# Kernel tuning notes

Hardware: AMD Instinct MI355X
Metric: run time of the kernel (lower is better)

The kernel has to match this reference:

```python
import jax, jax.numpy as jnp
import numpy as np

EPS = 1e-5
N_NODES = 50000


def batchnorm(x, gamma, beta):
    # training-mode BatchNorm1d: batch mean, biased variance
    mean = jnp.mean(x, axis=0)
    var = jnp.mean(jnp.square(x - mean), axis=0)
    return (x - mean) * jax.lax.rsqrt(var + EPS) * gamma + beta


def setup_inputs() -> dict:
    key = jax.random.key(0)
    ks = jax.random.split(key, 8)
    N, E, D_IN, D_H, D_OUT = N_NODES, 800000, 128, 128, 128
    feat = jax.random.normal(ks[0], (N, D_IN), dtype=jnp.float32)
    w = jax.random.uniform(ks[1], (E,), dtype=jnp.float32)
    # xavier_uniform with relu gain for Q and W
    gain = float(np.sqrt(2.0))
    bq = gain * np.sqrt(6.0 / (D_IN + D_H))
    bw = gain * np.sqrt(6.0 / (D_IN + D_H + D_OUT))
    Q_w = jax.random.uniform(ks[2], (D_H, D_IN), minval=-bq, maxval=bq, dtype=jnp.float32)
    W_w = jax.random.uniform(ks[3], (D_OUT, D_IN + D_H), minval=-bw, maxval=bw, dtype=jnp.float32)
    Q_b = jnp.zeros((D_H,), jnp.float32)
    W_b = jnp.zeros((D_OUT,), jnp.float32)
    gamma2 = jnp.ones((D_OUT,), jnp.float32)
    beta2 = jnp.zeros((D_OUT,), jnp.float32)
    src = jax.random.randint(ks[4], (E,), 0, N, dtype=jnp.int32)
    dst = jax.random.randint(ks[5], (E,), 0, N, dtype=jnp.int32)
    return {"feat": feat, "w": w, "Q_w": Q_w, "Q_b": Q_b, "W_w": W_w,
            "W_b": W_b, "gamma2": gamma2, "beta2": beta2, "src": src, "dst": dst}


def reference(feat, w, Q_w, Q_b, W_w, W_b, gamma2, beta2, src, dst):
    N = feat.shape[0]
    # h = dropout(bnorm_two(relu(Q(feat))))  (dropout=0 -> identity; source reuses bnorm_two)
    h = batchnorm(jax.nn.relu(feat @ Q_w.T + Q_b), gamma2, beta2)  # [N, H]
    # weighted neighbor mean: sum_e w_e * h[src_e] scattered to dst, / sum_e w_e
    num = jax.ops.segment_sum(w[:, None] * h[src], dst, num_segments=N)  # [N, H]
    den = jax.ops.segment_sum(w, dst, num_segments=N)  # [N]
    has_msg = den[:, None] != 0
    agg = jnp.where(has_msg, num / jnp.where(has_msg, den[:, None], 1.0), h)
    rst = jnp.concatenate([feat, agg], axis=1) @ W_w.T + W_b  # [N, OUT]
    rst = batchnorm(jax.nn.relu(rst), gamma2, beta2)
    denom = jnp.linalg.norm(rst, axis=1, keepdims=True)
    return rst / jnp.where(denom == 0, 1.0, denom)
```

## Files before the change

kernel.cpp:

```cpp
#include <hip/hip_runtime.h>
#include <stdint.h>


#define BN_EPS 1e-5f
#define NSLOT 32

typedef __attribute__((ext_vector_type(8))) short bf16x8;
typedef __attribute__((ext_vector_type(4))) float f32x4;

static __device__ __forceinline__ unsigned short f2bf(float f) {
    uint32_t u = __builtin_bit_cast(uint32_t, f);
    u += 0x7fffu + ((u >> 16) & 1u);
    return (unsigned short)(u >> 16);
}
static __device__ __forceinline__ float bf_lo(uint32_t u) {
    return __builtin_bit_cast(float, u << 16);
}
static __device__ __forceinline__ float bf_hi(uint32_t u) {
    return __builtin_bit_cast(float, u & 0xffff0000u);
}

__global__ __launch_bounds__(256) void k_pre(
    const float* __restrict__ feat, unsigned short* __restrict__ featb, int nf,
    const int* __restrict__ dst, int* __restrict__ ccnt, int E, int CB)
{
    if ((int)blockIdx.x < CB) {
        int i = (blockIdx.x * 256 + threadIdx.x) * 4;
        if (i + 3 < nf) {
            float4 v = *(const float4*)(feat + i);
            ushort4 o;
            o.x = f2bf(v.x); o.y = f2bf(v.y); o.z = f2bf(v.z); o.w = f2bf(v.w);
            *(ushort4*)(featb + i) = o;
        } else {
            for (int j = i; j < nf; ++j) featb[j] = f2bf(feat[j]);
        }
    } else {
        __shared__ int hcnt[128];
        const int tid = threadIdx.x;
        if (tid < 128) hcnt[tid] = 0;
        __syncthreads();
        const int base_e = (blockIdx.x - CB) * 2048;
#pragma unroll
        for (int j = 0; j < 8; ++j) {
            int e = base_e + j * 256 + tid;
            if (e < E) atomicAdd(&hcnt[dst[e] >> 9], 1);
        }
        __syncthreads();
        if (tid < 128 && hcnt[tid] > 0) atomicAdd(&ccnt[tid], hcnt[tid]);
    }
}

__global__ __launch_bounds__(128) void k_coffs(
    const int* __restrict__ ccnt, int* __restrict__ coffs,
    int* __restrict__ gcur, int* __restrict__ offs, int N, int E)
{
    __shared__ int w0sum;
    const int t = threadIdx.x;
    const int lane = t & 63, wv = t >> 6;
    int v = ccnt[t];
    int incl = v;
#pragma unroll
    for (int o = 1; o < 64; o <<= 1) {
        int u = __shfl_up(incl, o, 64);
        if (lane >= o) incl += u;
    }
    if (wv == 0 && lane == 63) w0sum = incl;
    __syncthreads();
    int excl = incl - v + (wv ? w0sum : 0);
    coffs[t] = excl;
    gcur[t]  = excl;
    if (t == 127) { coffs[128] = excl + v; offs[N] = E; }
}

template<int K>
static __device__ __forceinline__ void gemm_body(
    int bid,
    const unsigned short* __restrict__ A_lo,
    const unsigned short* __restrict__ A_hi,
    const float* __restrict__ B,
    const float* __restrict__ bias,
    float* __restrict__ Y,
    double* __restrict__ sum, double* __restrict__ sumsq, int N)
{
    constexpr int SA = 72;
    __shared__ unsigned short As[64 * SA];
    __shared__ unsigned short Bs[128 * SA];
    __shared__ float bsum_s[128], bsq_s[128];

    const int tid  = threadIdx.x;
    const int lane = tid & 63;
    const int wv   = tid >> 6;
    const int wr   = wv >> 1;
    const int wc   = wv & 1;
    const int m15  = lane & 15;
    const int quad = lane >> 4;
    const int r0   = bid * 64;

    if (tid < 128) { bsum_s[tid] = 0.f; bsq_s[tid] = 0.f; }

    f32x4 acc[2][4];
#pragma unroll
    for (int rt = 0; rt < 2; ++rt)
#pragma unroll
        for (int ct = 0; ct < 4; ++ct)
            acc[rt][ct] = (f32x4){0.f, 0.f, 0.f, 0.f};

    for (int kc = 0; kc < K; kc += 64) {
        const unsigned short* Ap = (kc < 128) ? A_lo : A_hi;
        const int koff = kc & 127;
#pragma unroll
        for (int i = 0; i < 2; ++i) {
            int idx = i * 256 + tid;
            int row = idx >> 3, seg = idx & 7;
            int gr  = r0 + row; if (gr >= N) gr = N - 1;
            uint4 v = *(const uint4*)(Ap + (size_t)gr * 128 + koff + seg * 8);
            *(uint4*)(As + row * SA + seg * 8) = v;
        }
#pragma unroll
        for (int i = 0; i < 8; ++i) {
            int idx = i * 256 + tid;
            int row = idx >> 4, seg = idx & 15;
            float4 v = *(const float4*)(B + (size_t)row * K + kc + seg * 4);
            ushort4 o;
            o.x = f2bf(v.x); o.y = f2bf(v.y); o.z = f2bf(v.z); o.w = f2bf(v.w);
            *(ushort4*)(Bs + row * SA + seg * 4) = o;
        }
        __syncthreads();

#pragma unroll
        for (int ks = 0; ks < 64; ks += 32) {
            bf16x8 af[2], bfr[4];
#pragma unroll
            for (int rt = 0; rt < 2; ++rt)
                af[rt] = *(const bf16x8*)(As + (wr * 32 + rt * 16 + m15) * SA + ks + quad * 8);
#pragma unroll
            for (int ct = 0; ct < 4; ++ct)
                bfr[ct] = *(const bf16x8*)(Bs + (wc * 64 + ct * 16 + m15) * SA + ks + quad * 8);
#pragma unroll
            for (int rt = 0; rt < 2; ++rt)
#pragma unroll
                for (int ct = 0; ct < 4; ++ct)
                    acc[rt][ct] = __builtin_amdgcn_mfma_f32_16x16x32_bf16(
                        af[rt], bfr[ct], acc[rt][ct], 0, 0, 0);
        }
        __syncthreads();
    }

#pragma unroll
    for (int ct = 0; ct < 4; ++ct) {
        int col = wc * 64 + ct * 16 + m15;
        float bz = bias[col];
        float s = 0.f, q = 0.f;
#pragma unroll
        for (int rt = 0; rt < 2; ++rt) {
#pragma unroll
            for (int reg = 0; reg < 4; ++reg) {
                int row = r0 + wr * 32 + rt * 16 + quad * 4 + reg;
                float v = fmaxf(acc[rt][ct][reg] + bz, 0.f);
                if (row < N) {
                    Y[(size_t)row * 128 + col] = v;
                } else {
                    v = 0.f;
                }
                s += v; q = fmaf(v, v, q);
            }
        }
        s += __shfl_xor(s, 16, 64); s += __shfl_xor(s, 32, 64);
        q += __shfl_xor(q, 16, 64); q += __shfl_xor(q, 32, 64);
        if (quad == 0) {
            atomicAdd(&bsum_s[col], s);
            atomicAdd(&bsq_s[col], q);
        }
    }
    __syncthreads();
    if (tid < 128) {
        const int slot = (bid & (NSLOT - 1)) * 128;
        atomicAdd(&sum[slot + tid],   (double)bsum_s[tid]);
        atomicAdd(&sumsq[slot + tid], (double)bsq_s[tid]);
    }
}

static __device__ __forceinline__ void bin_body(
    int bid,
    const int* __restrict__ src, const int* __restrict__ dst,
    const float* __restrict__ w, int* __restrict__ gcur,
    int4* __restrict__ tmp, int E)
{
    __shared__ int hcnt[128];
    __shared__ int hbase[128];
    const int tid = threadIdx.x;
    if (tid < 128) hcnt[tid] = 0;
    __syncthreads();

    int d8[8], s8[8], slot8[8];
    float w8[8];
#pragma unroll
    for (int j = 0; j < 8; ++j) {
        int e = bid * 2048 + j * 256 + tid;
        if (e < E) {
            d8[j] = dst[e]; s8[j] = src[e]; w8[j] = w[e];
            slot8[j] = atomicAdd(&hcnt[d8[j] >> 9], 1);
        } else d8[j] = -1;
    }
    __syncthreads();
    if (tid < 128 && hcnt[tid] > 0)
        hbase[tid] = atomicAdd(&gcur[tid], hcnt[tid]);
    __syncthreads();
#pragma unroll
    for (int j = 0; j < 8; ++j) {
        if (d8[j] >= 0) {
            int pos = hbase[d8[j] >> 9] + slot8[j];
            tmp[pos] = make_int4(s8[j], __float_as_int(w8[j]), d8[j], 0);
        }
    }
}

__global__ __launch_bounds__(256) void k_bin_gemm(
    const int* __restrict__ src, const int* __restrict__ dst,
    const float* __restrict__ w, int* __restrict__ gcur,
    int4* __restrict__ tmp, int E, int HB,
    const unsigned short* __restrict__ featb,
    const float* __restrict__ Qw, const float* __restrict__ Qb,
    float* __restrict__ y1,
    double* __restrict__ sum, double* __restrict__ sumsq, int N)
{
    if ((int)blockIdx.x < HB)
        bin_body(blockIdx.x, src, dst, w, gcur, tmp, E);
    else
        gemm_body<128>(blockIdx.x - HB, featb, featb, Qw, Qb, y1, sum, sumsq, N);
}

__global__ __launch_bounds__(128) void bn_coef(
    const double* __restrict__ sum, const double* __restrict__ sumsq,
    const float* __restrict__ gamma, const float* __restrict__ beta,
    float* __restrict__ a, float* __restrict__ b, double invN)
{
    const int t = threadIdx.x;
    double ms = 0.0, qs = 0.0;
#pragma unroll
    for (int s = 0; s < NSLOT; ++s) {
        ms += sum[s * 128 + t];
        qs += sumsq[s * 128 + t];
    }
    float mean = (float)(ms * invN);
    float var  = (float)(qs * invN) - mean * mean;
    float sc = rsqrtf(var + BN_EPS) * gamma[t];
    a[t] = sc;
    b[t] = fmaf(-mean, sc, beta[t]);
}

static __device__ __forceinline__ void refine_body(
    int b,
    const int4* __restrict__ tmp, const int* __restrict__ coffs,
    int* __restrict__ offs, int2* __restrict__ epack, int N)
{
    __shared__ int hist[512];
    __shared__ int wpre[4];
    const int d0   = b << 9;
    const int dlim = min(512, N - d0);
    const int tid  = threadIdx.x;
    const int lane = tid & 63, wv = tid >> 6;
    const int start = coffs[b];
    const int end   = coffs[b + 1];

    hist[tid] = 0; hist[tid + 256] = 0;
    __syncthreads();

    for (int p = start + tid; p < end; p += 256)
        atomicAdd(&hist[tmp[p].z - d0], 1);
    __syncthreads();

    int v0 = hist[2 * tid], v1 = hist[2 * tid + 1];
    int s = v0 + v1;
    int incl = s;
#pragma unroll
    for (int o = 1; o < 64; o <<= 1) {
        int t = __shfl_up(incl, o, 64);
        if (lane >= o) incl += t;
    }
    if (lane == 63) wpre[wv] = incl;
    __syncthreads();
    if (tid == 0) {
        int r = 0;
#pragma unroll
        for (int i = 0; i < 4; ++i) { int t = wpre[i]; wpre[i] = r; r += t; }
    }
    __syncthreads();
    int e0 = start + wpre[wv] + incl - s;
    if (2 * tid < dlim)     offs[d0 + 2 * tid]     = e0;
    if (2 * tid + 1 < dlim) offs[d0 + 2 * tid + 1] = e0 + v0;
    hist[2 * tid]     = e0;
    hist[2 * tid + 1] = e0 + v0;
    __syncthreads();

    for (int p = start + tid; p < end; p += 256) {
        int4 rec = tmp[p];
        int pos = atomicAdd(&hist[rec.z - d0], 1);
        epack[pos] = make_int2(rec.x, rec.y);
    }
}

__global__ __launch_bounds__(256) void k_refine_apply(
    const int4* __restrict__ tmp, const int* __restrict__ coffs,
    int* __restrict__ offs, int2* __restrict__ epack, int N, int NB,
    const float* __restrict__ y,
    const float* __restrict__ a, const float* __restrict__ b,
    unsigned short* __restrict__ h, int n)
{
    if ((int)blockIdx.x < NB) {
        refine_body(blockIdx.x, tmp, coffs, offs, epack, N);
    } else {
        int i = ((blockIdx.x - NB) * 256 + threadIdx.x) * 4;
        if (i >= n) return;
        int c = i & 127;
        float4 v  = *(const float4*)(y + i);
        float4 av = *(const float4*)(a + c);
        float4 bv = *(const float4*)(b + c);
        ushort4 o;
        o.x = f2bf(fmaf(av.x, v.x, bv.x));
        o.y = f2bf(fmaf(av.y, v.y, bv.y));
        o.z = f2bf(fmaf(av.z, v.z, bv.z));
        o.w = f2bf(fmaf(av.w, v.w, bv.w));
        *(ushort4*)(h + i) = o;
    }
}

__global__ __launch_bounds__(256) void gather_agg(
    const unsigned short* __restrict__ h,
    const int* __restrict__ offs, const int2* __restrict__ epack,
    unsigned short* __restrict__ aggb, int N)
{
    const int r    = (int)((blockIdx.x * 256u + threadIdx.x) >> 6);
    const int lane = threadIdx.x & 63;
    if (r >= N) return;
    int p = offs[r];
    const int end = offs[r + 1];
    float nx = 0.f, ny = 0.f, den = 0.f;
    for (; p + 3 < end; p += 4) {
        int2 e0 = epack[p],     e1 = epack[p + 1];
        int2 e2 = epack[p + 2], e3 = epack[p + 3];
        uint32_t u0 = *(const uint32_t*)(h + (size_t)e0.x * 128 + 2 * lane);
        uint32_t u1 = *(const uint32_t*)(h + (size_t)e1.x * 128 + 2 * lane);
        uint32_t u2 = *(const uint32_t*)(h + (size_t)e2.x * 128 + 2 * lane);
        uint32_t u3 = *(const uint32_t*)(h + (size_t)e3.x * 128 + 2 * lane);
        float w0 = __int_as_float(e0.y), w1 = __int_as_float(e1.y);
        float w2 = __int_as_float(e2.y), w3 = __int_as_float(e3.y);
        nx = fmaf(w0, bf_lo(u0), nx); ny = fmaf(w0, bf_hi(u0), ny);
        nx = fmaf(w1, bf_lo(u1), nx); ny = fmaf(w1, bf_hi(u1), ny);
        nx = fmaf(w2, bf_lo(u2), nx); ny = fmaf(w2, bf_hi(u2), ny);
        nx = fmaf(w3, bf_lo(u3), nx); ny = fmaf(w3, bf_hi(u3), ny);
        den += (w0 + w1) + (w2 + w3);
    }
    for (; p < end; ++p) {
        int2 e0 = epack[p];
        float w0 = __int_as_float(e0.y);
        uint32_t u0 = *(const uint32_t*)(h + (size_t)e0.x * 128 + 2 * lane);
        nx = fmaf(w0, bf_lo(u0), nx); ny = fmaf(w0, bf_hi(u0), ny);
        den += w0;
    }
    float2 outv;
    if (den != 0.f) {
        float inv = 1.f / den;
        outv.x = nx * inv; outv.y = ny * inv;
    } else {
        uint32_t u = *(const uint32_t*)(h + (size_t)r * 128 + 2 * lane);
        outv.x = bf_lo(u); outv.y = bf_hi(u);
    }
    ushort2 ao; ao.x = f2bf(outv.x); ao.y = f2bf(outv.y);
    *(ushort2*)&aggb[(size_t)r * 128 + 2 * lane] = ao;
}

__global__ __launch_bounds__(256) void gemm_bn2(
    const unsigned short* __restrict__ A_lo,
    const unsigned short* __restrict__ A_hi,
    const float* __restrict__ B,
    const float* __restrict__ bias,
    float* __restrict__ Y,
    double* __restrict__ sum, double* __restrict__ sumsq, int N)
{
    gemm_body<256>(blockIdx.x, A_lo, A_hi, B, bias, Y, sum, sumsq, N);
}

__global__ __launch_bounds__(256) void finalize(
    const float* __restrict__ Y2,
    const float* __restrict__ a, const float* __restrict__ b,
    float* __restrict__ out, int N)
{
    __shared__ float sa[128], sb[128];
    const int t = threadIdx.x;
    if (t < 128) { sa[t] = a[t]; sb[t] = b[t]; }
    __syncthreads();
    const int row  = (int)((blockIdx.x * 256u + t) >> 6);
    const int lane = t & 63;
    if (row >= N) return;
    const size_t base = (size_t)row * 128;
    float v0 = fmaf(sa[lane],      Y2[base + lane],      sb[lane]);
    float v1 = fmaf(sa[lane + 64], Y2[base + lane + 64], sb[lane + 64]);
    float ss = fmaf(v0, v0, v1 * v1);
#pragma unroll
    for (int o = 32; o; o >>= 1) ss += __shfl_xor(ss, o, 64);
    float nrm = sqrtf(ss);
    float inv = (nrm == 0.f) ? 1.f : 1.f / nrm;
    out[base + lane]      = v0 * inv;
    out[base + lane + 64] = v1 * inv;
}

extern "C" void kernel_launch(void* const* d_in, const int* in_sizes, int n_in,
                              void* d_out, int out_size, void* d_ws, size_t ws_size,
                              hipStream_t stream)
{
    const float* feat   = (const float*)d_in[0];
    const float* w      = (const float*)d_in[1];
    const float* Q_w    = (const float*)d_in[2];
    const float* Q_b    = (const float*)d_in[3];
    const float* W_w    = (const float*)d_in[4];
    const float* W_b    = (const float*)d_in[5];
    const float* gamma2 = (const float*)d_in[6];
    const float* beta2  = (const float*)d_in[7];
    const int*   src    = (const int*)d_in[8];
    const int*   dst    = (const int*)d_in[9];

    const int N = in_sizes[0] / 128;
    const int E = in_sizes[1];

    float*          y1    = (float*)d_ws;
    unsigned short* featb = (unsigned short*)(y1 + (size_t)N * 128);
    unsigned short* aggb  = featb + (size_t)N * 128;
    unsigned short* h_bf  = aggb + (size_t)N * 128;
    int4*  tmp    = (int4*)(h_bf + (size_t)N * 128);
    int2*  epack  = (int2*)(tmp + E);
    int*   offs   = (int*)(epack + E);
    int*   coffs  = offs + (N + 1);
    int*   gcur   = coffs + 129;
    float* coefs  = (float*)(gcur + 128);
    float* a1 = coefs, *b1 = coefs + 128, *a2 = coefs + 256, *b2 = coefs + 384;
    uintptr_t sp  = ((uintptr_t)(coefs + 512) + 7) & ~(uintptr_t)7;
    double* stats = (double*)sp;
    double* sum1   = stats;
    double* sumsq1 = stats + NSLOT * 128;
    double* sum2   = stats + 2 * NSLOT * 128;
    double* sumsq2 = stats + 3 * NSLOT * 128;
    int*   ccnt   = (int*)(stats + 4 * NSLOT * 128);

    hipMemsetAsync(stats, 0,
                   4 * NSLOT * 128 * sizeof(double) + 128 * sizeof(int),
                   stream);

    const double invN = 1.0 / (double)N;
    const int GB = (N + 63) / 64;
    const int NB = (N + 511) >> 9;
    const int CB = (N * 128 / 4 + 255) / 256;
    const int HB = (E + 2047) / 2048;
    const int AB = (N * 128 / 4 + 255) / 256;

    k_pre<<<CB + HB, 256, 0, stream>>>(feat, featb, N * 128, dst, ccnt, E, CB);
    k_coffs<<<1, 128, 0, stream>>>(ccnt, coffs, gcur, offs, N, E);

    k_bin_gemm<<<HB + GB, 256, 0, stream>>>(
        src, dst, w, gcur, tmp, E, HB,
        featb, Q_w, Q_b, y1, sum1, sumsq1, N);
    bn_coef<<<1, 128, 0, stream>>>(sum1, sumsq1, gamma2, beta2, a1, b1, invN);

    k_refine_apply<<<NB + AB, 256, 0, stream>>>(
        tmp, coffs, offs, epack, N, NB,
        y1, a1, b1, h_bf, N * 128);

    gather_agg<<<(N * 64 + 255) / 256, 256, 0, stream>>>(h_bf, offs, epack, aggb, N);

    gemm_bn2<<<GB, 256, 0, stream>>>(
        featb, aggb, W_w, W_b, y1 , sum2, sumsq2, N);
    bn_coef<<<1, 128, 0, stream>>>(sum2, sumsq2, gamma2, beta2, a2, b2, invN);
    finalize<<<(N * 64 + 255) / 256, 256, 0, stream>>>(
        y1, a2, b2, (float*)d_out, N);
}
```

Baseline: 244.8 us.

## Fold scan and BN-coef kernels into last-block epilogues, pre-cast weights to bf16

Drops the separate k_coffs and bn_coef launches. The last finishing block, detected with an atomic counter, now does the prefix scan inside k_pre and the BN coefficient reduction inside each GEMM. Q_w and W_w are cast to bf16 once in k_pre instead of being converted in every GEMM block. The GEMM also drops the LDS staging and loads MFMA fragments directly from global memory. This removes three small launches and the redundant weight conversion, at the risk of uncoalesced direct loads and the extra fences and counters.

New measurement: 401.2 us. 63.9% more time.

```diff
diff --git a/kernel.cpp b/kernel.cpp
--- a/kernel.cpp
+++ b/kernel.cpp
@@ -20,56 +20,77 @@
     return __builtin_bit_cast(float, u & 0xffff0000u);
 }
 
+static __device__ __forceinline__ void cast_blk(
+    const float* __restrict__ src, unsigned short* __restrict__ dst,
+    int n, int blk)
+{
+    int i = (blk * 256 + threadIdx.x) * 4;
+    if (i + 3 < n) {
+        float4 v = *(const float4*)(src + i);
+        ushort4 o;
+        o.x = f2bf(v.x); o.y = f2bf(v.y); o.z = f2bf(v.z); o.w = f2bf(v.w);
+        *(ushort4*)(dst + i) = o;
+    } else {
+        for (int j = i; j < n; ++j) dst[j] = f2bf(src[j]);
+    }
+}
+
 __global__ __launch_bounds__(256) void k_pre(
     const float* __restrict__ feat, unsigned short* __restrict__ featb, int nf,
-    const int* __restrict__ dst, int* __restrict__ ccnt, int E, int CB)
-{
-    if ((int)blockIdx.x < CB) {
-        int i = (blockIdx.x * 256 + threadIdx.x) * 4;
-        if (i + 3 < nf) {
-            float4 v = *(const float4*)(feat + i);
-            ushort4 o;
-            o.x = f2bf(v.x); o.y = f2bf(v.y); o.z = f2bf(v.z); o.w = f2bf(v.w);
-            *(ushort4*)(featb + i) = o;
-        } else {
-            for (int j = i; j < nf; ++j) featb[j] = f2bf(feat[j]);
+    const int* __restrict__ dst, int* __restrict__ ccnt, int E, int CB, int HB,
+    const float* __restrict__ Qw, unsigned short* __restrict__ Qwb,
+    const float* __restrict__ Ww, unsigned short* __restrict__ Wwb,
+    int* __restrict__ done, int* __restrict__ coffs, int* __restrict__ gcur,
+    int* __restrict__ offs, int N)
+{
+    int b = (int)blockIdx.x;
+    if (b < CB) { cast_blk(feat, featb, nf, b); return; }
+    b -= CB;
+    if (b >= HB) {
+        b -= HB;
+        if (b < 16) cast_blk(Qw, Qwb, 128 * 128, b);
+        else        cast_blk(Ww, Wwb, 128 * 256, b - 16);
+        return;
+    }
+    __shared__ int hcnt[128];
+    __shared__ bool last;
+    const int tid = threadIdx.x;
+    if (tid < 128) hcnt[tid] = 0;
+    __syncthreads();
+    const int base_e = b * 2048;
+#pragma unroll
+    for (int j = 0; j < 8; ++j) {
+        int e = base_e + j * 256 + tid;
+        if (e < E) atomicAdd(&hcnt[dst[e] >> 9], 1);
+    }
+    __syncthreads();
+    if (tid < 128 && hcnt[tid] > 0) atomicAdd(&ccnt[tid], hcnt[tid]);
+    __threadfence();
+    __syncthreads();
+    if (tid == 0) last = (atomicAdd(&done[0], 1) == HB - 1);
+    __syncthreads();
+    if (!last) return;
+    __threadfence();
+    __shared__ int w0sum;
+    int v = 0, incl = 0;
+    if (tid < 128) {
+        v = __hip_atomic_load(&ccnt[tid], __ATOMIC_RELAXED, __HIP_MEMORY_SCOPE_AGENT);
+        incl = v;
+        const int lane = tid & 63;
+#pragma unroll
+        for (int o = 1; o < 64; o <<= 1) {
+            int u = __shfl_up(incl, o, 64);
+            if (lane >= o) incl += u;
         }
-    } else {
-        __shared__ int hcnt[128];
-        const int tid = threadIdx.x;
-        if (tid < 128) hcnt[tid] = 0;
-        __syncthreads();
-        const int base_e = (blockIdx.x - CB) * 2048;
-#pragma unroll
-        for (int j = 0; j < 8; ++j) {
-            int e = base_e + j * 256 + tid;
-            if (e < E) atomicAdd(&hcnt[dst[e] >> 9], 1);
-        }
-        __syncthreads();
-        if (tid < 128 && hcnt[tid] > 0) atomicAdd(&ccnt[tid], hcnt[tid]);
-    }
-}
-
-__global__ __launch_bounds__(128) void k_coffs(
-    const int* __restrict__ ccnt, int* __restrict__ coffs,
-    int* __restrict__ gcur, int* __restrict__ offs, int N, int E)
-{
-    __shared__ int w0sum;
-    const int t = threadIdx.x;
-    const int lane = t & 63, wv = t >> 6;
-    int v = ccnt[t];
-    int incl = v;
-#pragma unroll
-    for (int o = 1; o < 64; o <<= 1) {
-        int u = __shfl_up(incl, o, 64);
-        if (lane >= o) incl += u;
-    }
-    if (wv == 0 && lane == 63) w0sum = incl;
-    __syncthreads();
-    int excl = incl - v + (wv ? w0sum : 0);
-    coffs[t] = excl;
-    gcur[t]  = excl;
-    if (t == 127) { coffs[128] = excl + v; offs[N] = E; }
+        if (tid == 63) w0sum = incl;
+    }
+    __syncthreads();
+    if (tid < 128) {
+        int excl = incl - v + ((tid >> 6) ? w0sum : 0);
+        coffs[tid] = excl;
+        gcur[tid]  = excl;
+        if (tid == 127) { coffs[128] = excl + v; offs[N] = E; }
+    }
 }
 
 template<int K>
@@ -77,15 +98,16 @@
     int bid,
     const unsigned short* __restrict__ A_lo,
     const unsigned short* __restrict__ A_hi,
-    const float* __restrict__ B,
+    const unsigned short* __restrict__ Bb,
     const float* __restrict__ bias,
     float* __restrict__ Y,
-    double* __restrict__ sum, double* __restrict__ sumsq, int N)
-{
-    constexpr int SA = 72;
-    __shared__ unsigned short As[64 * SA];
-    __shared__ unsigned short Bs[128 * SA];
+    double* __restrict__ sum, double* __restrict__ sumsq, int N,
+    int* __restrict__ done, int nblk,
+    const float* __restrict__ gamma, const float* __restrict__ beta,
+    float* __restrict__ a, float* __restrict__ b, double invN)
+{
     __shared__ float bsum_s[128], bsq_s[128];
+    __shared__ bool lastblk;
 
     const int tid  = threadIdx.x;
     const int lane = tid & 63;
@@ -98,6 +120,13 @@
 
     if (tid < 128) { bsum_s[tid] = 0.f; bsq_s[tid] = 0.f; }
 
+    int ra0 = r0 + wr * 32 + m15;      if (ra0 >= N) ra0 = N - 1;
+    int ra1 = r0 + wr * 32 + 16 + m15; if (ra1 >= N) ra1 = N - 1;
+    const unsigned short* br0 = Bb + (size_t)(wc * 64 +  0 + m15) * K;
+    const unsigned short* br1 = Bb + (size_t)(wc * 64 + 16 + m15) * K;
+    const unsigned short* br2 = Bb + (size_t)(wc * 64 + 32 + m15) * K;
+    const unsigned short* br3 = Bb + (size_t)(wc * 64 + 48 + m15) * K;
+
     f32x4 acc[2][4];
 #pragma unroll
     for (int rt = 0; rt < 2; ++rt)
@@ -105,46 +134,28 @@
         for (int ct = 0; ct < 4; ++ct)
             acc[rt][ct] = (f32x4){0.f, 0.f, 0.f, 0.f};
 
-    for (int kc = 0; kc < K; kc += 64) {
+#pragma unroll
+    for (int kc = 0; kc < K; kc += 32) {
         const unsigned short* Ap = (kc < 128) ? A_lo : A_hi;
-        const int koff = kc & 127;
-#pragma unroll
-        for (int i = 0; i < 2; ++i) {
-            int idx = i * 256 + tid;
-            int row = idx >> 3, seg = idx & 7;
-            int gr  = r0 + row; if (gr >= N) gr = N - 1;
-            uint4 v = *(const uint4*)(Ap + (size_t)gr * 128 + koff + seg * 8);
-            *(uint4*)(As + row * SA + seg * 8) = v;
-        }
-#pragma unroll
-        for (int i = 0; i < 8; ++i) {
-            int idx = i * 256 + tid;
-            int row = idx >> 4, seg = idx & 15;
-            float4 v = *(const float4*)(B + (size_t)row * K + kc + seg * 4);
-            ushort4 o;
-            o.x = f2bf(v.x); o.y = f2bf(v.y); o.z = f2bf(v.z); o.w = f2bf(v.w);
-            *(ushort4*)(Bs + row * SA + seg * 4) = o;
-        }
-        __syncthreads();
-
-#pragma unroll
-        for (int ks = 0; ks < 64; ks += 32) {
-            bf16x8 af[2], bfr[4];
-#pragma unroll
-            for (int rt = 0; rt < 2; ++rt)
-                af[rt] = *(const bf16x8*)(As + (wr * 32 + rt * 16 + m15) * SA + ks + quad * 8);
-#pragma unroll
-            for (int ct = 0; ct < 4; ++ct)
-                bfr[ct] = *(const bf16x8*)(Bs + (wc * 64 + ct * 16 + m15) * SA + ks + quad * 8);
-#pragma unroll
-            for (int rt = 0; rt < 2; ++rt)
-#pragma unroll
-                for (int ct = 0; ct < 4; ++ct)
-                    acc[rt][ct] = __builtin_amdgcn_mfma_f32_16x16x32_bf16(
-                        af[rt], bfr[ct], acc[rt][ct], 0, 0, 0);
-        }
-        __syncthreads();
-    }
+        const int ko = (kc & 127) + quad * 8;
+        const int kb = kc + quad * 8;
+        bf16x8 af0 = *(const bf16x8*)(Ap + (size_t)ra0 * 128 + ko);
+        bf16x8 af1 = *(const bf16x8*)(Ap + (size_t)ra1 * 128 + ko);
+        bf16x8 b0  = *(const bf16x8*)(br0 + kb);
+        bf16x8 b1  = *(const bf16x8*)(br1 + kb);
+        bf16x8 b2  = *(const bf16x8*)(br2 + kb);
+        bf16x8 b3  = *(const bf16x8*)(br3 + kb);
+        acc[0][0] = __builtin_amdgcn_mfma_f32_16x16x32_bf16(af0, b0, acc[0][0], 0, 0, 0);
+        acc[1][0] = __builtin_amdgcn_mfma_f32_16x16x32_bf16(af1, b0, acc[1][0], 0, 0, 0);
+        acc[0][1] = __builtin_amdgcn_mfma_f32_16x16x32_bf16(af0, b1, acc[0][1], 0, 0, 0);
+        acc[1][1] = __builtin_amdgcn_mfma_f32_16x16x32_bf16(af1, b1, acc[1][1], 0, 0, 0);
+        acc[0][2] = __builtin_amdgcn_mfma_f32_16x16x32_bf16(af0, b2, acc[0][2], 0, 0, 0);
+        acc[1][2] = __builtin_amdgcn_mfma_f32_16x16x32_bf16(af1, b2, acc[1][2], 0, 0, 0);
+        acc[0][3] = __builtin_amdgcn_mfma_f32_16x16x32_bf16(af0, b3, acc[0][3], 0, 0, 0);
+        acc[1][3] = __builtin_amdgcn_mfma_f32_16x16x32_bf16(af1, b3, acc[1][3], 0, 0, 0);
+    }
+
+    __syncthreads();
 
 #pragma unroll
     for (int ct = 0; ct < 4; ++ct) {
@@ -156,13 +167,13 @@
 #pragma unroll
             for (int reg = 0; reg < 4; ++reg) {
                 int row = r0 + wr * 32 + rt * 16 + quad * 4 + reg;
-                float v = fmaxf(acc[rt][ct][reg] + bz, 0.f);
+                float vv = fmaxf(acc[rt][ct][reg] + bz, 0.f);
                 if (row < N) {
-                    Y[(size_t)row * 128 + col] = v;
+                    Y[(size_t)row * 128 + col] = vv;
                 } else {
-                    v = 0.f;
+                    vv = 0.f;
                 }
-                s += v; q = fmaf(v, v, q);
+                s += vv; q = fmaf(vv, vv, q);
             }
         }
         s += __shfl_xor(s, 16, 64); s += __shfl_xor(s, 32, 64);
@@ -178,6 +189,23 @@
         atomicAdd(&sum[slot + tid],   (double)bsum_s[tid]);
         atomicAdd(&sumsq[slot + tid], (double)bsq_s[tid]);
     }
+    __threadfence();
+    __syncthreads();
+    if (tid == 0) lastblk = (atomicAdd(done, 1) == nblk - 1);
+    __syncthreads();
+    if (lastblk && tid < 128) {
+        double ms = 0.0, qs = 0.0;
+#pragma unroll
+        for (int s2 = 0; s2 < NSLOT; ++s2) {
+            ms += __hip_atomic_load(&sum[s2 * 128 + tid],   __ATOMIC_RELAXED, __HIP_MEMORY_SCOPE_AGENT);
+            qs += __hip_atomic_load(&sumsq[s2 * 128 + tid], __ATOMIC_RELAXED, __HIP_MEMORY_SCOPE_AGENT);
+        }
+        float mean = (float)(ms * invN);
+        float var  = (float)(qs * invN) - mean * mean;
+        float sc = rsqrtf(var + BN_EPS) * gamma[tid];
+        a[tid] = sc;
+        b[tid] = fmaf(-mean, sc, beta[tid]);
+    }
 }
 
 static __device__ __forceinline__ void bin_body(
@@ -220,33 +248,18 @@
     const float* __restrict__ w, int* __restrict__ gcur,
     int4* __restrict__ tmp, int E, int HB,
     const unsigned short* __restrict__ featb,
-    const float* __restrict__ Qw, const float* __restrict__ Qb,
+    const unsigned short* __restrict__ Qwb, const float* __restrict__ Qb,
     float* __restrict__ y1,
-    double* __restrict__ sum, double* __restrict__ sumsq, int N)
+    double* __restrict__ sum, double* __restrict__ sumsq, int N,
+    int* __restrict__ done, int GB,
+    const float* __restrict__ gamma, const float* __restrict__ beta,
+    float* __restrict__ a, float* __restrict__ b, double invN)
 {
     if ((int)blockIdx.x < HB)
         bin_body(blockIdx.x, src, dst, w, gcur, tmp, E);
     else
-        gemm_body<128>(blockIdx.x - HB, featb, featb, Qw, Qb, y1, sum, sumsq, N);
-}
-
-__global__ __launch_bounds__(128) void bn_coef(
-    const double* __restrict__ sum, const double* __restrict__ sumsq,
-    const float* __restrict__ gamma, const float* __restrict__ beta,
-    float* __restrict__ a, float* __restrict__ b, double invN)
-{
-    const int t = threadIdx.x;
-    double ms = 0.0, qs = 0.0;
-#pragma unroll
-    for (int s = 0; s < NSLOT; ++s) {
-        ms += sum[s * 128 + t];
-        qs += sumsq[s * 128 + t];
-    }
-    float mean = (float)(ms * invN);
-    float var  = (float)(qs * invN) - mean * mean;
-    float sc = rsqrtf(var + BN_EPS) * gamma[t];
-    a[t] = sc;
-    b[t] = fmaf(-mean, sc, beta[t]);
+        gemm_body<128>(blockIdx.x - HB, featb, featb, Qwb, Qb, y1, sum, sumsq, N,
+                       done, GB, gamma, beta, a, b, invN);
 }
 
 static __device__ __forceinline__ void refine_body(
@@ -373,12 +386,16 @@
 __global__ __launch_bounds__(256) void gemm_bn2(
     const unsigned short* __restrict__ A_lo,
     const unsigned short* __restrict__ A_hi,
-    const float* __restrict__ B,
+    const unsigned short* __restrict__ Bb,
     const float* __restrict__ bias,
     float* __restrict__ Y,
-    double* __restrict__ sum, double* __restrict__ sumsq, int N)
-{
-    gemm_body<256>(blockIdx.x, A_lo, A_hi, B, bias, Y, sum, sumsq, N);
+    double* __restrict__ sum, double* __restrict__ sumsq, int N,
+    int* __restrict__ done, int GB,
+    const float* __restrict__ gamma, const float* __restrict__ beta,
+    float* __restrict__ a, float* __restrict__ b, double invN)
+{
+    gemm_body<256>(blockIdx.x, A_lo, A_hi, Bb, bias, Y, sum, sumsq, N,
+                   done, GB, gamma, beta, a, b, invN);
 }
 
 __global__ __launch_bounds__(256) void finalize(
@@ -434,16 +451,20 @@
     int*   gcur   = coffs + 129;
     float* coefs  = (float*)(gcur + 128);
     float* a1 = coefs, *b1 = coefs + 128, *a2 = coefs + 256, *b2 = coefs + 384;
-    uintptr_t sp  = ((uintptr_t)(coefs + 512) + 7) & ~(uintptr_t)7;
+    uintptr_t qp = ((uintptr_t)(coefs + 512) + 15) & ~(uintptr_t)15;
+    unsigned short* Qwb = (unsigned short*)qp;
+    unsigned short* Wwb = Qwb + 128 * 128;
+    uintptr_t sp = ((uintptr_t)(Wwb + 128 * 256) + 15) & ~(uintptr_t)15;
     double* stats = (double*)sp;
     double* sum1   = stats;
     double* sumsq1 = stats + NSLOT * 128;
     double* sum2   = stats + 2 * NSLOT * 128;
     double* sumsq2 = stats + 3 * NSLOT * 128;
     int*   ccnt   = (int*)(stats + 4 * NSLOT * 128);
+    int*   done   = ccnt + 128;
 
     hipMemsetAsync(stats, 0,
-                   4 * NSLOT * 128 * sizeof(double) + 128 * sizeof(int),
+                   4 * NSLOT * 128 * sizeof(double) + 132 * sizeof(int),
                    stream);
 
     const double invN = 1.0 / (double)N;
@@ -452,14 +473,17 @@
     const int CB = (N * 128 / 4 + 255) / 256;
     const int HB = (E + 2047) / 2048;
     const int AB = (N * 128 / 4 + 255) / 256;
-
-    k_pre<<<CB + HB, 256, 0, stream>>>(feat, featb, N * 128, dst, ccnt, E, CB);
-    k_coffs<<<1, 128, 0, stream>>>(ccnt, coffs, gcur, offs, N, E);
+    const int QB = 16;
+    const int WB = 32;
+
+    k_pre<<<CB + HB + QB + WB, 256, 0, stream>>>(
+        feat, featb, N * 128, dst, ccnt, E, CB, HB,
+        Q_w, Qwb, W_w, Wwb, done, coffs, gcur, offs, N);
 
     k_bin_gemm<<<HB + GB, 256, 0, stream>>>(
         src, dst, w, gcur, tmp, E, HB,
-        featb, Q_w, Q_b, y1, sum1, sumsq1, N);
-    bn_coef<<<1, 128, 0, stream>>>(sum1, sumsq1, gamma2, beta2, a1, b1, invN);
+        featb, Qwb, Q_b, y1, sum1, sumsq1, N,
+        done + 1, GB, gamma2, beta2, a1, b1, invN);
 
     k_refine_apply<<<NB + AB, 256, 0, stream>>>(
         tmp, coffs, offs, epack, N, NB,
@@ -468,8 +492,9 @@
     gather_agg<<<(N * 64 + 255) / 256, 256, 0, stream>>>(h_bf, offs, epack, aggb, N);
 
     gemm_bn2<<<GB, 256, 0, stream>>>(
-        featb, aggb, W_w, W_b, y1 , sum2, sumsq2, N);
-    bn_coef<<<1, 128, 0, stream>>>(sum2, sumsq2, gamma2, beta2, a2, b2, invN);
+        featb, aggb, Wwb, W_b, y1 , sum2, sumsq2, N,
+        done + 2, GB, gamma2, beta2, a2, b2, invN);
+
     finalize<<<(N * 64 + 255) / 256, 256, 0, stream>>>(
         y1, a2, b2, (float*)d_out, N);
 }
```
